# Optimization experiments

Hardware: AMD Instinct MI355X
Metric: run time of the kernel (lower is better)

## Reference

```python
import jax, jax.numpy as jnp
import numpy as np

N_NODES = 100000
N_EDGES = 1600000
N_GRAPHS = 256
F_IN = 128
NEURON = 64
AF = 8  # attention_num_feature


def gcn_conv(h_in, W, b, src, dst, n):
    # PyG GCNConv: add self loops, symmetric normalization, XW then aggregate, + bias
    h = h_in @ W  # [N, out]
    loop = jnp.arange(n)
    s = jnp.concatenate([src, loop])
    d = jnp.concatenate([dst, loop])
    deg = jax.ops.segment_sum(jnp.ones(s.shape[0], h.dtype), d, num_segments=n)
    dis = jax.lax.rsqrt(deg)  # deg >= 1 because of self loops
    norm = dis[s] * dis[d]  # [E+N]
    msg = h[s] * norm[:, None]
    out = jax.ops.segment_sum(msg, d, num_segments=n)
    return out + b


def setup_inputs() -> dict:
    key = jax.random.key(0)
    ks = jax.random.split(key, 16)
    x = jax.random.normal(ks[0], (N_NODES, F_IN), dtype=jnp.float32)
    closeness = jax.random.normal(ks[1], (N_NODES, AF), dtype=jnp.float32)
    edge_index = jax.random.randint(ks[2], (2, N_EDGES), 0, N_NODES, dtype=jnp.int64)
    batch = jnp.sort(jax.random.randint(ks[3], (N_NODES,), 0, N_GRAPHS, dtype=jnp.int64))
    def lin(k, fi, fo):
        lim = 1.0 / np.sqrt(fi)
        return jax.random.uniform(k, (fi, fo), jnp.float32, -lim, lim)
    return {
        "x": x, "closeness": closeness,
        "W1": lin(ks[4], F_IN, NEURON), "b1": jnp.zeros((NEURON,), jnp.float32),
        "W2": lin(ks[5], NEURON, NEURON), "b2": jnp.zeros((NEURON,), jnp.float32),
        "W3": lin(ks[6], NEURON, NEURON), "b3": jnp.zeros((NEURON,), jnp.float32),
        "Wc": lin(ks[7], AF, 1), "bc": jnp.zeros((1,), jnp.float32),
        "Wa1": lin(ks[8], NEURON, 16), "ba1": jnp.zeros((16,), jnp.float32),
        "Wa2": lin(ks[9], 16, 1), "ba2": jnp.zeros((1,), jnp.float32),
        "edge_index": edge_index, "batch": batch,
    }


def reference(x, closeness, W1, b1, W2, b2, W3, b3, Wc, bc, Wa1, ba1, Wa2, ba2, edge_index, batch):
    n, G = x.shape[0], N_GRAPHS
    src, dst = edge_index[0], edge_index[1]
    h = jax.nn.relu(gcn_conv(x, W1, b1, src, dst, n))
    h = jax.nn.relu(gcn_conv(h, W2, b2, src, dst, n))
    h = jax.nn.relu(gcn_conv(h, W3, b3, src, dst, n))  # [N, 64]
    # per-graph softmax over closeness logits (vectorized form of the python loop)
    logits = (closeness @ Wc + bc)[:, 0]  # [N]
    m = jax.ops.segment_max(logits, batch, num_segments=G)
    e = jnp.exp(logits - m[batch])
    z = jax.ops.segment_sum(e, batch, num_segments=G)
    p = e / z[batch]  # softmax within each graph
    counts = jax.ops.segment_sum(jnp.ones((n,), h.dtype), batch, num_segments=G)
    counts = jnp.maximum(counts, 1.0)
    attn = p * counts[batch]  # softmax * curr_size
    # self_average: mean over nodes of attn * h  == segment_sum / count
    g = jax.ops.segment_sum(attn[:, None] * h, batch, num_segments=G) / counts[:, None]  # [G, 64]
    a = jax.nn.relu(g @ Wa1 + ba1)
    return a @ Wa2 + ba2  # [G, 1]
```

## Files before the change

### kernel.cpp

```cpp
#include <hip/hip_runtime.h>
#include <hip/hip_fp16.h>
#include <math.h>


#define BKT_SHIFT 7
#define BKT_NODES 128
#define BKT_CAP 4096
#define EPB 8192

__global__ __launch_bounds__(1024) void block_hist_kernel(
    const int* __restrict__ dst, int* __restrict__ hist, int E, int NBKT, int NBLK) {
  __shared__ int lh[1024];
  const int t = threadIdx.x;
  const int blk = blockIdx.x;
  for (int k = t; k < NBKT; k += 1024) lh[k] = 0;
  __syncthreads();
  const int e0 = blk * EPB;
  const int e1 = min(e0 + EPB, E);
  for (int e = e0 + t; e < e1; e += 1024) atomicAdd(&lh[dst[e] >> BKT_SHIFT], 1);
  __syncthreads();
  for (int k = t; k < NBKT; k += 1024) hist[k * NBLK + blk] = lh[k];
}

__global__ __launch_bounds__(256) void row_scan_kernel(
    const int* __restrict__ hist, int* __restrict__ ebase, int* __restrict__ btot,
    int NBLK) {
  __shared__ int sh[256];
  const int k = blockIdx.x;
  const int t = threadIdx.x;
  int v = (t < NBLK) ? hist[(long)k * NBLK + t] : 0;
  sh[t] = v;
  __syncthreads();
  for (int s = 1; s < 256; s <<= 1) {
    int add = (t >= s) ? sh[t - s] : 0;
    __syncthreads();
    sh[t] += add;
    __syncthreads();
  }
  if (t < NBLK) ebase[(long)k * NBLK + t] = sh[t] - v;
  if (t == 255) btot[k] = sh[255];
}

__global__ __launch_bounds__(1024) void bucket_scan_kernel(
    const int* __restrict__ btot, int* __restrict__ bbase, int E, int NBKT) {
  __shared__ int sh[1024];
  const int t = threadIdx.x;
  int v = (t < NBKT) ? btot[t] : 0;
  sh[t] = v;
  __syncthreads();
  for (int s = 1; s < 1024; s <<= 1) {
    int add = (t >= s) ? sh[t - s] : 0;
    __syncthreads();
    sh[t] += add;
    __syncthreads();
  }
  if (t < NBKT) bbase[t] = sh[t] - v;
  if (t == 0) bbase[NBKT] = E;
}

__global__ __launch_bounds__(1024) void group_kernel(
    const int* __restrict__ src, const int* __restrict__ dst,
    const int* __restrict__ bbase, const int* __restrict__ ebase,
    unsigned int* __restrict__ grouped, int E, int NBKT, int NBLK) {
  __shared__ int lcur[1024];
  const int t = threadIdx.x;
  const int blk = blockIdx.x;
  for (int k = t; k < NBKT; k += 1024)
    lcur[k] = bbase[k] + ebase[(long)k * NBLK + blk];
  __syncthreads();
  const int e0 = blk * EPB;
  const int e1 = min(e0 + EPB, E);
  for (int e = e0 + t; e < e1; e += 1024) {
    int d = dst[e];
    int b = d >> BKT_SHIFT;
    int pos = atomicAdd(&lcur[b], 1);
    grouped[pos] = ((unsigned int)(d & (BKT_NODES - 1)) << 17) | (unsigned int)src[e];
  }
}

__global__ __launch_bounds__(256) void bucket_build_kernel(
    const unsigned int* __restrict__ grouped, const int* __restrict__ bbase,
    int* __restrict__ csr_src, int* __restrict__ ends, float* __restrict__ dis, int N) {
  __shared__ int lcnt[BKT_NODES];
  __shared__ int lsum[BKT_NODES];
  __shared__ int lcur[BKT_NODES];
  __shared__ int stage[BKT_CAP];
  const int b = blockIdx.x;
  const int t = threadIdx.x;
  const int node0 = b << BKT_SHIFT;
  const int nn = min(BKT_NODES, N - node0);
  const int base = bbase[b];
  const int m = bbase[b + 1] - base;

  if (t < BKT_NODES) lcnt[t] = 0;
  __syncthreads();
  for (int i = t; i < m; i += 256) atomicAdd(&lcnt[grouped[base + i] >> 17], 1);
  __syncthreads();
  if (t < BKT_NODES) lsum[t] = lcnt[t];
  __syncthreads();
  for (int s = 1; s < BKT_NODES; s <<= 1) {
    int add = 0;
    if (t < BKT_NODES && t >= s) add = lsum[t - s];
    __syncthreads();
    if (t < BKT_NODES) lsum[t] += add;
    __syncthreads();
  }
  if (t < nn) {
    ends[node0 + t] = base + lsum[t];
    dis[node0 + t] = 1.0f / sqrtf((float)(lcnt[t] + 1));
    lcur[t] = lsum[t] - lcnt[t];
  }
  __syncthreads();
  if (m <= BKT_CAP) {
    for (int i = t; i < m; i += 256) {
      unsigned int v = grouped[base + i];
      int p = atomicAdd(&lcur[v >> 17], 1);
      stage[p] = (int)(v & 0x1FFFFu);
    }
    __syncthreads();
    for (int i = t; i < m; i += 256) csr_src[base + i] = stage[i];
  } else {
    for (int i = t; i < m; i += 256) {
      unsigned int v = grouped[base + i];
      int p = atomicAdd(&lcur[v >> 17], 1);
      csr_src[base + p] = (int)(v & 0x1FFFFu);
    }
  }
}


template <int K>
__global__ __launch_bounds__(256) void gemm_kernel(const float* __restrict__ H,
                                                   const float* __restrict__ W,
                                                   const float* __restrict__ dis,
                                                   __half* __restrict__ C, int N) {
  __shared__ float Hs[64][68];
  __shared__ float Ws[64][64];
  const int t = threadIdx.x;
  const int rowBase = blockIdx.x * 64;
  const int cg = t & 7, pr = t >> 3;
  const int c0 = cg * 8, r0 = pr * 2;
  float acc0[8] = {0.f, 0.f, 0.f, 0.f, 0.f, 0.f, 0.f, 0.f};
  float acc1[8] = {0.f, 0.f, 0.f, 0.f, 0.f, 0.f, 0.f, 0.f};

  const int sr = t >> 4, sc4 = (t & 15) * 4;

  for (int k0 = 0; k0 < K; k0 += 64) {
    __syncthreads();
    {
      const float4* Wv = reinterpret_cast<const float4*>(W + (long)k0 * 64);
#pragma unroll
      for (int i = 0; i < 4; ++i) {
        int idx = t + i * 256;
        *reinterpret_cast<float4*>(&Ws[idx >> 4][(idx & 15) * 4]) = Wv[idx];
      }
    }
#pragma unroll
    for (int i = 0; i < 4; ++i) {
      int r = sr + i * 16;
      int gr = rowBase + r;
      float4 v = make_float4(0.f, 0.f, 0.f, 0.f);
      if (gr < N) v = *reinterpret_cast<const float4*>(H + (long)gr * K + k0 + sc4);
      *reinterpret_cast<float4*>(&Hs[r][sc4]) = v;
    }
    __syncthreads();
#pragma unroll 4
    for (int kk = 0; kk < 64; kk += 4) {
      float4 h0 = *reinterpret_cast<const float4*>(&Hs[r0][kk]);
      float4 h1 = *reinterpret_cast<const float4*>(&Hs[r0 + 1][kk]);
#pragma unroll
      for (int j = 0; j < 4; ++j) {
        float hj0 = (&h0.x)[j];
        float hj1 = (&h1.x)[j];
        const float4 w0 = *reinterpret_cast<const float4*>(&Ws[kk + j][c0]);
        const float4 w1 = *reinterpret_cast<const float4*>(&Ws[kk + j][c0 + 4]);
        acc0[0] += hj0 * w0.x; acc0[1] += hj0 * w0.y; acc0[2] += hj0 * w0.z; acc0[3] += hj0 * w0.w;
        acc0[4] += hj0 * w1.x; acc0[5] += hj0 * w1.y; acc0[6] += hj0 * w1.z; acc0[7] += hj0 * w1.w;
        acc1[0] += hj1 * w0.x; acc1[1] += hj1 * w0.y; acc1[2] += hj1 * w0.z; acc1[3] += hj1 * w0.w;
        acc1[4] += hj1 * w1.x; acc1[5] += hj1 * w1.y; acc1[6] += hj1 * w1.z; acc1[7] += hj1 * w1.w;
      }
    }
  }
  int gr0 = rowBase + r0;
  if (gr0 < N) {
    float s = dis[gr0];
    union { uint4 u; __half2 h[4]; } pk;
    pk.h[0] = __floats2half2_rn(acc0[0] * s, acc0[1] * s);
    pk.h[1] = __floats2half2_rn(acc0[2] * s, acc0[3] * s);
    pk.h[2] = __floats2half2_rn(acc0[4] * s, acc0[5] * s);
    pk.h[3] = __floats2half2_rn(acc0[6] * s, acc0[7] * s);
    *reinterpret_cast<uint4*>(&C[(long)gr0 * 64 + c0]) = pk.u;
  }
  if (gr0 + 1 < N) {
    float s = dis[gr0 + 1];
    union { uint4 u; __half2 h[4]; } pk;
    pk.h[0] = __floats2half2_rn(acc1[0] * s, acc1[1] * s);
    pk.h[1] = __floats2half2_rn(acc1[2] * s, acc1[3] * s);
    pk.h[2] = __floats2half2_rn(acc1[4] * s, acc1[5] * s);
    pk.h[3] = __floats2half2_rn(acc1[6] * s, acc1[7] * s);
    *reinterpret_cast<uint4*>(&C[(long)(gr0 + 1) * 64 + c0]) = pk.u;
  }
}


__device__ __forceinline__ float4 h4_to_f4(uint2 u) {
  const __half2 lo = *reinterpret_cast<const __half2*>(&u.x);
  const __half2 hi = *reinterpret_cast<const __half2*>(&u.y);
  const float2 flo = __half22float2(lo);
  const float2 fhi = __half22float2(hi);
  return make_float4(flo.x, flo.y, fhi.x, fhi.y);
}

__global__ __launch_bounds__(256) void aggregate_kernel(
    const __half* __restrict__ Ts, const int* __restrict__ csr_src,
    const int* __restrict__ ends, const float* __restrict__ dis,
    const float* __restrict__ bias, float* __restrict__ O, int N) {
  int gid = blockIdx.x * 256 + threadIdx.x;
  int d = gid >> 6;
  if (d >= N) return;
  const int lane = threadIdx.x & 63;
  const int q = lane >> 4;
  const int c = lane & 15;
  const int beg = (d == 0) ? 0 : ends[d - 1];
  const int m = ends[d] - beg;
  const uint2* Tv = (const uint2*)Ts;
  const int* sl = csr_src + beg;

  float4 a0 = make_float4(0.f, 0.f, 0.f, 0.f);
  float4 a1 = a0, a2 = a0, a3 = a0;
  if (q == 0) a0 = h4_to_f4(Tv[(long)d * 16 + c]);

  for (int base = 0; base < m; base += 64) {
    const int take = min(m - base, 64);
    int idx = (lane < take) ? sl[base + lane] : 0;
    for (int j = 0; j < take; j += 16) {
      const int l0 = j + q, l1 = j + 4 + q, l2 = j + 8 + q, l3 = j + 12 + q;
      int s0 = __shfl(idx, l0 & 63, 64);
      int s1 = __shfl(idx, l1 & 63, 64);
      int s2 = __shfl(idx, l2 & 63, 64);
      int s3 = __shfl(idx, l3 & 63, 64);
      uint2 r0 = Tv[(long)s0 * 16 + c];
      uint2 r1 = Tv[(long)s1 * 16 + c];
      uint2 r2 = Tv[(long)s2 * 16 + c];
      uint2 r3 = Tv[(long)s3 * 16 + c];
      if (l0 < take) { float4 f = h4_to_f4(r0); a0.x += f.x; a0.y += f.y; a0.z += f.z; a0.w += f.w; }
      if (l1 < take) { float4 f = h4_to_f4(r1); a1.x += f.x; a1.y += f.y; a1.z += f.z; a1.w += f.w; }
      if (l2 < take) { float4 f = h4_to_f4(r2); a2.x += f.x; a2.y += f.y; a2.z += f.z; a2.w += f.w; }
      if (l3 < take) { float4 f = h4_to_f4(r3); a3.x += f.x; a3.y += f.y; a3.z += f.z; a3.w += f.w; }
    }
  }
  a0.x += a1.x; a0.y += a1.y; a0.z += a1.z; a0.w += a1.w;
  a2.x += a3.x; a2.y += a3.y; a2.z += a3.z; a2.w += a3.w;
  a0.x += a2.x; a0.y += a2.y; a0.z += a2.z; a0.w += a2.w;

  a0.x += __shfl_xor(a0.x, 16, 64); a0.y += __shfl_xor(a0.y, 16, 64);
  a0.z += __shfl_xor(a0.z, 16, 64); a0.w += __shfl_xor(a0.w, 16, 64);
  a0.x += __shfl_xor(a0.x, 32, 64); a0.y += __shfl_xor(a0.y, 32, 64);
  a0.z += __shfl_xor(a0.z, 32, 64); a0.w += __shfl_xor(a0.w, 32, 64);

  if (q == 0) {
    float dd = dis[d];
    float4 b4 = ((const float4*)bias)[c];
    float4 o;
    o.x = fmaxf(a0.x * dd + b4.x, 0.f);
    o.y = fmaxf(a0.y * dd + b4.y, 0.f);
    o.z = fmaxf(a0.z * dd + b4.z, 0.f);
    o.w = fmaxf(a0.w * dd + b4.w, 0.f);
    ((float4*)O)[(long)d * 16 + c] = o;
  }
}


__global__ void logits_kernel(const float* __restrict__ clo, const float* __restrict__ Wc,
                              const float* __restrict__ bc, float* __restrict__ lb, int N) {
  int i = blockIdx.x * blockDim.x + threadIdx.x;
  if (i >= N) return;
  float s = bc[0];
#pragma unroll
  for (int k = 0; k < 8; ++k) s += clo[(long)i * 8 + k] * Wc[k];
  lb[i] = s;
}

__global__ __launch_bounds__(256) void pool_kernel(
    const float* __restrict__ h3, const float* __restrict__ lb,
    const int* __restrict__ batch, const float* __restrict__ Wa1,
    const float* __restrict__ ba1, const float* __restrict__ Wa2,
    const float* __restrict__ ba2, float* __restrict__ out, int N) {
  __shared__ int sLo, sHi;
  __shared__ float red[256];
  __shared__ float Vs[4][64];
  __shared__ float sse[4];
  __shared__ float gv[64];
  __shared__ float am[16];
  const int g = blockIdx.x;
  const int t = threadIdx.x;
  if (t == 0) {
    int lo = 0, hi = N;
    while (lo < hi) { int mid = (lo + hi) >> 1; if (batch[mid] < g) lo = mid + 1; else hi = mid; }
    sLo = lo;
    lo = 0; hi = N;
    while (lo < hi) { int mid = (lo + hi) >> 1; if (batch[mid] < g + 1) lo = mid + 1; else hi = mid; }
    sHi = lo;
  }
  __syncthreads();
  const int lo = sLo, hi = sHi;

  float lm = -1e30f;
  for (int i = lo + t; i < hi; i += 256) lm = fmaxf(lm, lb[i]);
  red[t] = lm;
  __syncthreads();
  for (int s = 128; s > 0; s >>= 1) {
    if (t < s) red[t] = fmaxf(red[t], red[t + s]);
    __syncthreads();
  }
  const float m = red[0];

  const int f = t & 63, sub = t >> 6;
  float vacc = 0.f, seacc = 0.f;
  for (int i = lo + sub; i < hi; i += 4) {
    float e = expf(lb[i] - m);
    seacc += e;
    vacc += e * h3[(long)i * 64 + f];
  }
  Vs[sub][f] = vacc;
  if (f == 0) sse[sub] = seacc;
  __syncthreads();
  if (t < 64) {
    float se = sse[0] + sse[1] + sse[2] + sse[3];
    float v = Vs[0][f] + Vs[1][f] + Vs[2][f] + Vs[3][f];
    gv[f] = (se > 0.f) ? v / se : 0.f;
  }
  __syncthreads();
  if (t < 16) {
    float a = ba1[t];
#pragma unroll
    for (int k2 = 0; k2 < 64; ++k2) a += gv[k2] * Wa1[k2 * 16 + t];
    am[t] = a > 0.f ? a : 0.f;
  }
  __syncthreads();
  if (t == 0) {
    float o = ba2[0];
#pragma unroll
    for (int j = 0; j < 16; ++j) o += am[j] * Wa2[j];
    out[g] = o;
  }
}


extern "C" void kernel_launch(void* const* d_in, const int* in_sizes, int n_in,
                              void* d_out, int out_size, void* d_ws, size_t ws_size,
                              hipStream_t stream) {
  const float* x   = (const float*)d_in[0];
  const float* clo = (const float*)d_in[1];
  const float* W1  = (const float*)d_in[2];
  const float* b1  = (const float*)d_in[3];
  const float* W2  = (const float*)d_in[4];
  const float* b2  = (const float*)d_in[5];
  const float* W3  = (const float*)d_in[6];
  const float* b3  = (const float*)d_in[7];
  const float* Wc  = (const float*)d_in[8];
  const float* bc  = (const float*)d_in[9];
  const float* Wa1 = (const float*)d_in[10];
  const float* ba1 = (const float*)d_in[11];
  const float* Wa2 = (const float*)d_in[12];
  const float* ba2 = (const float*)d_in[13];
  const int* edge  = (const int*)d_in[14];
  const int* batch = (const int*)d_in[15];
  float* out = (float*)d_out;

  const int N = in_sizes[15];
  const int E = in_sizes[14] / 2;
  const int G = out_size;
  const int NBKT = (N + BKT_NODES - 1) >> BKT_SHIFT;
  const int NBLK = (E + EPB - 1) / EPB;

  const int* src = edge;
  const int* dst = edge + E;

  char* p = (char*)d_ws;
  auto alloc = [&](size_t bytes) -> char* {
    char* r = p;
    p += (bytes + 255) & ~(size_t)255;
    return r;
  };
  __half* tsbuf         = (__half*)alloc((size_t)N * 64 * sizeof(__half));
  float* bufB           = (float*)alloc((size_t)N * 64 * sizeof(float));
  int*   csr_src        = (int*)  alloc((size_t)E * sizeof(int));
  unsigned int* grouped = (unsigned int*)alloc((size_t)E * sizeof(unsigned int));
  int*   hist           = (int*)  alloc((size_t)NBKT * NBLK * sizeof(int));
  int*   ebase          = (int*)  alloc((size_t)NBKT * NBLK * sizeof(int));
  int*   btot           = (int*)  alloc((size_t)NBKT * sizeof(int));
  int*   bbase          = (int*)  alloc((size_t)(NBKT + 1) * sizeof(int));
  int*   ends           = (int*)  alloc((size_t)N * sizeof(int));
  float* dis            = (float*)alloc((size_t)N * sizeof(float));
  float* lb             = (float*)alloc((size_t)N * sizeof(float));
  (void)ws_size; (void)n_in;

  block_hist_kernel<<<NBLK, 1024, 0, stream>>>(dst, hist, E, NBKT, NBLK);
  row_scan_kernel<<<NBKT, 256, 0, stream>>>(hist, ebase, btot, NBLK);
  bucket_scan_kernel<<<1, 1024, 0, stream>>>(btot, bbase, E, NBKT);
  group_kernel<<<NBLK, 1024, 0, stream>>>(src, dst, bbase, ebase, grouped, E, NBKT, NBLK);
  bucket_build_kernel<<<NBKT, 256, 0, stream>>>(grouped, bbase, csr_src, ends, dis, N);

  const int gN = (N + 255) / 256;
  const int gGemm = (N + 63) / 64;
  const int gAgg  = (N * 64 + 255) / 256;

  gemm_kernel<128><<<gGemm, 256, 0, stream>>>(x, W1, dis, tsbuf, N);
  aggregate_kernel<<<gAgg, 256, 0, stream>>>(tsbuf, csr_src, ends, dis, b1, bufB, N);
  gemm_kernel<64><<<gGemm, 256, 0, stream>>>(bufB, W2, dis, tsbuf, N);
  aggregate_kernel<<<gAgg, 256, 0, stream>>>(tsbuf, csr_src, ends, dis, b2, bufB, N);
  gemm_kernel<64><<<gGemm, 256, 0, stream>>>(bufB, W3, dis, tsbuf, N);
  aggregate_kernel<<<gAgg, 256, 0, stream>>>(tsbuf, csr_src, ends, dis, b3, bufB, N);

  logits_kernel<<<gN, 256, 0, stream>>>(clo, Wc, bc, lb, N);
  pool_kernel<<<G, 256, 0, stream>>>(bufB, lb, batch, Wa1, ba1, Wa2, ba2, out, N);
}
```

Measured before the change: 377.2 us.

## Use MFMA fp16 GEMM and store intermediate activations in half precision

New measurement: 352.0 us. -6.7%, faster.

```diff
diff --git a/kernel.cpp b/kernel.cpp
--- a/kernel.cpp
+++ b/kernel.cpp
@@ -7,6 +7,9 @@
 #define BKT_NODES 128
 #define BKT_CAP 4096
 #define EPB 8192
+
+typedef _Float16 f16x8 __attribute__((ext_vector_type(8)));
+typedef float f32x4 __attribute__((ext_vector_type(4)));
 
 __global__ __launch_bounds__(1024) void block_hist_kernel(
     const int* __restrict__ dst, int* __restrict__ hist, int E, int NBKT, int NBLK) {
@@ -129,76 +132,102 @@
 }
 
 
-template <int K>
-__global__ __launch_bounds__(256) void gemm_kernel(const float* __restrict__ H,
-                                                   const float* __restrict__ W,
-                                                   const float* __restrict__ dis,
-                                                   __half* __restrict__ C, int N) {
-  __shared__ float Hs[64][68];
-  __shared__ float Ws[64][64];
+template <int K, typename Tin>
+__global__ __launch_bounds__(256) void gemm_mfma_kernel(
+    const Tin* __restrict__ H, const float* __restrict__ W,
+    const float* __restrict__ dis, __half* __restrict__ C, int N) {
+  __shared__ __align__(16) __half Hs[64 * K];
+  __shared__ __align__(16) __half Ws[64 * K];
   const int t = threadIdx.x;
   const int rowBase = blockIdx.x * 64;
-  const int cg = t & 7, pr = t >> 3;
-  const int c0 = cg * 8, r0 = pr * 2;
-  float acc0[8] = {0.f, 0.f, 0.f, 0.f, 0.f, 0.f, 0.f, 0.f};
-  float acc1[8] = {0.f, 0.f, 0.f, 0.f, 0.f, 0.f, 0.f, 0.f};
-
-  const int sr = t >> 4, sc4 = (t & 15) * 4;
-
-  for (int k0 = 0; k0 < K; k0 += 64) {
-    __syncthreads();
-    {
-      const float4* Wv = reinterpret_cast<const float4*>(W + (long)k0 * 64);
-#pragma unroll
-      for (int i = 0; i < 4; ++i) {
-        int idx = t + i * 256;
-        *reinterpret_cast<float4*>(&Ws[idx >> 4][(idx & 15) * 4]) = Wv[idx];
+
+  if constexpr (sizeof(Tin) == 4) {
+    const int NF4 = 64 * K / 4;
+#pragma unroll
+    for (int i = 0; i < NF4 / 256; ++i) {
+      int f = t + i * 256;
+      int row = f / (K / 4);
+      int c4 = f % (K / 4);
+      int gr = rowBase + row;
+      float4 v = make_float4(0.f, 0.f, 0.f, 0.f);
+      if (gr < N) v = *reinterpret_cast<const float4*>(H + (long)gr * K + c4 * 4);
+      union { uint2 u; __half2 h[2]; } pk;
+      pk.h[0] = __floats2half2_rn(v.x, v.y);
+      pk.h[1] = __floats2half2_rn(v.z, v.w);
+      int byte = (row * K + c4 * 4) * 2;
+      byte ^= (row & 7) << 4;
+      *reinterpret_cast<uint2*>(reinterpret_cast<char*>(Hs) + byte) = pk.u;
+    }
+  } else {
+    const int NC = 64 * K / 8;
+#pragma unroll
+    for (int i = 0; i < NC / 256; ++i) {
+      int f = t + i * 256;
+      int row = f / (K / 8);
+      int c8 = f % (K / 8);
+      int gr = rowBase + row;
+      uint4 v = make_uint4(0u, 0u, 0u, 0u);
+      if (gr < N) v = *reinterpret_cast<const uint4*>(H + (long)gr * K + c8 * 8);
+      int byte = (row * K + c8 * 8) * 2;
+      byte ^= (row & 7) << 4;
+      *reinterpret_cast<uint4*>(reinterpret_cast<char*>(Hs) + byte) = v;
+    }
+  }
+
+  {
+    const int NU = (K / 2) * 16;
+#pragma unroll
+    for (int i = 0; i < NU / 256; ++i) {
+      int u = t + i * 256;
+      int kp = u >> 4;
+      int cq = u & 15;
+      const float4 w0 = *reinterpret_cast<const float4*>(W + (long)(2 * kp) * 64 + cq * 4);
+      const float4 w1 = *reinterpret_cast<const float4*>(W + (long)(2 * kp + 1) * 64 + cq * 4);
+#pragma unroll
+      for (int j = 0; j < 4; ++j) {
+        int c = cq * 4 + j;
+        __half2 p = __floats2half2_rn((&w0.x)[j], (&w1.x)[j]);
+        int byte = (c * K + 2 * kp) * 2;
+        byte ^= (c & 7) << 4;
+        *reinterpret_cast<__half2*>(reinterpret_cast<char*>(Ws) + byte) = p;
       }
     }
-#pragma unroll
-    for (int i = 0; i < 4; ++i) {
-      int r = sr + i * 16;
-      int gr = rowBase + r;
-      float4 v = make_float4(0.f, 0.f, 0.f, 0.f);
-      if (gr < N) v = *reinterpret_cast<const float4*>(H + (long)gr * K + k0 + sc4);
-      *reinterpret_cast<float4*>(&Hs[r][sc4]) = v;
-    }
-    __syncthreads();
-#pragma unroll 4
-    for (int kk = 0; kk < 64; kk += 4) {
-      float4 h0 = *reinterpret_cast<const float4*>(&Hs[r0][kk]);
-      float4 h1 = *reinterpret_cast<const float4*>(&Hs[r0 + 1][kk]);
-#pragma unroll
-      for (int j = 0; j < 4; ++j) {
-        float hj0 = (&h0.x)[j];
-        float hj1 = (&h1.x)[j];
-        const float4 w0 = *reinterpret_cast<const float4*>(&Ws[kk + j][c0]);
-        const float4 w1 = *reinterpret_cast<const float4*>(&Ws[kk + j][c0 + 4]);
-        acc0[0] += hj0 * w0.x; acc0[1] += hj0 * w0.y; acc0[2] += hj0 * w0.z; acc0[3] += hj0 * w0.w;
-        acc0[4] += hj0 * w1.x; acc0[5] += hj0 * w1.y; acc0[6] += hj0 * w1.z; acc0[7] += hj0 * w1.w;
-        acc1[0] += hj1 * w0.x; acc1[1] += hj1 * w0.y; acc1[2] += hj1 * w0.z; acc1[3] += hj1 * w0.w;
-        acc1[4] += hj1 * w1.x; acc1[5] += hj1 * w1.y; acc1[6] += hj1 * w1.z; acc1[7] += hj1 * w1.w;
+  }
+  __syncthreads();
+
+  const int w = t >> 6;
+  const int l = t & 63;
+  const int r = l & 15;
+  const int g = l >> 4;
+  const int rowL = 16 * w + r;
+  f32x4 acc[4] = {{0.f, 0.f, 0.f, 0.f}, {0.f, 0.f, 0.f, 0.f},
+                  {0.f, 0.f, 0.f, 0.f}, {0.f, 0.f, 0.f, 0.f}};
+#pragma unroll
+  for (int s = 0; s < K / 32; ++s) {
+    int abyte = (rowL * K + s * 32 + g * 8) * 2;
+    abyte ^= (rowL & 7) << 4;
+    f16x8 afrag = *reinterpret_cast<const f16x8*>(reinterpret_cast<const char*>(Hs) + abyte);
+#pragma unroll
+    for (int n = 0; n < 4; ++n) {
+      int col = n * 16 + r;
+      int bbyte = (col * K + s * 32 + g * 8) * 2;
+      bbyte ^= (col & 7) << 4;
+      f16x8 bfrag = *reinterpret_cast<const f16x8*>(reinterpret_cast<const char*>(Ws) + bbyte);
+      acc[n] = __builtin_amdgcn_mfma_f32_16x16x32_f16(afrag, bfrag, acc[n], 0, 0, 0);
+    }
+  }
+
+  const int outRow0 = rowBase + 16 * w + 4 * g;
+#pragma unroll
+  for (int j = 0; j < 4; ++j) {
+    int row = outRow0 + j;
+    if (row < N) {
+      float dv = dis[row];
+#pragma unroll
+      for (int n = 0; n < 4; ++n) {
+        C[(long)row * 64 + n * 16 + r] = __float2half(acc[n][j] * dv);
       }
     }
-  }
-  int gr0 = rowBase + r0;
-  if (gr0 < N) {
-    float s = dis[gr0];
-    union { uint4 u; __half2 h[4]; } pk;
-    pk.h[0] = __floats2half2_rn(acc0[0] * s, acc0[1] * s);
-    pk.h[1] = __floats2half2_rn(acc0[2] * s, acc0[3] * s);
-    pk.h[2] = __floats2half2_rn(acc0[4] * s, acc0[5] * s);
-    pk.h[3] = __floats2half2_rn(acc0[6] * s, acc0[7] * s);
-    *reinterpret_cast<uint4*>(&C[(long)gr0 * 64 + c0]) = pk.u;
-  }
-  if (gr0 + 1 < N) {
-    float s = dis[gr0 + 1];
-    union { uint4 u; __half2 h[4]; } pk;
-    pk.h[0] = __floats2half2_rn(acc1[0] * s, acc1[1] * s);
-    pk.h[1] = __floats2half2_rn(acc1[2] * s, acc1[3] * s);
-    pk.h[2] = __floats2half2_rn(acc1[4] * s, acc1[5] * s);
-    pk.h[3] = __floats2half2_rn(acc1[6] * s, acc1[7] * s);
-    *reinterpret_cast<uint4*>(&C[(long)(gr0 + 1) * 64 + c0]) = pk.u;
   }
 }
 
@@ -214,7 +243,7 @@
 __global__ __launch_bounds__(256) void aggregate_kernel(
     const __half* __restrict__ Ts, const int* __restrict__ csr_src,
     const int* __restrict__ ends, const float* __restrict__ dis,
-    const float* __restrict__ bias, float* __restrict__ O, int N) {
+    const float* __restrict__ bias, __half* __restrict__ O, int N) {
   int gid = blockIdx.x * 256 + threadIdx.x;
   int d = gid >> 6;
   if (d >= N) return;
@@ -261,12 +290,10 @@
   if (q == 0) {
     float dd = dis[d];
     float4 b4 = ((const float4*)bias)[c];
-    float4 o;
-    o.x = fmaxf(a0.x * dd + b4.x, 0.f);
-    o.y = fmaxf(a0.y * dd + b4.y, 0.f);
-    o.z = fmaxf(a0.z * dd + b4.z, 0.f);
-    o.w = fmaxf(a0.w * dd + b4.w, 0.f);
-    ((float4*)O)[(long)d * 16 + c] = o;
+    union { uint2 u; __half2 h[2]; } pk;
+    pk.h[0] = __floats2half2_rn(fmaxf(a0.x * dd + b4.x, 0.f), fmaxf(a0.y * dd + b4.y, 0.f));
+    pk.h[1] = __floats2half2_rn(fmaxf(a0.z * dd + b4.z, 0.f), fmaxf(a0.w * dd + b4.w, 0.f));
+    ((uint2*)O)[(long)d * 16 + c] = pk.u;
   }
 }
 
@@ -282,7 +309,7 @@
 }
 
 __global__ __launch_bounds__(256) void pool_kernel(
-    const float* __restrict__ h3, const float* __restrict__ lb,
+    const __half* __restrict__ h3, const float* __restrict__ lb,
     const int* __restrict__ batch, const float* __restrict__ Wa1,
     const float* __restrict__ ba1, const float* __restrict__ Wa2,
     const float* __restrict__ ba2, float* __restrict__ out, int N) {
@@ -320,7 +347,7 @@
   for (int i = lo + sub; i < hi; i += 4) {
     float e = expf(lb[i] - m);
     seacc += e;
-    vacc += e * h3[(long)i * 64 + f];
+    vacc += e * __half2float(h3[(long)i * 64 + f]);
   }
   Vs[sub][f] = vacc;
   if (f == 0) sse[sub] = seacc;
@@ -384,7 +411,7 @@
     return r;
   };
   __half* tsbuf         = (__half*)alloc((size_t)N * 64 * sizeof(__half));
-  float* bufB           = (float*)alloc((size_t)N * 64 * sizeof(float));
+  __half* bufH          = (__half*)alloc((size_t)N * 64 * sizeof(__half));
   int*   csr_src        = (int*)  alloc((size_t)E * sizeof(int));
   unsigned int* grouped = (unsigned int*)alloc((size_t)E * sizeof(unsigned int));
   int*   hist           = (int*)  alloc((size_t)NBKT * NBLK * sizeof(int));
@@ -406,13 +433,13 @@
   const int gGemm = (N + 63) / 64;
   const int gAgg  = (N * 64 + 255) / 256;
 
-  gemm_kernel<128><<<gGemm, 256, 0, stream>>>(x, W1, dis, tsbuf, N);
-  aggregate_kernel<<<gAgg, 256, 0, stream>>>(tsbuf, csr_src, ends, dis, b1, bufB, N);
-  gemm_kernel<64><<<gGemm, 256, 0, stream>>>(bufB, W2, dis, tsbuf, N);
-  aggregate_kernel<<<gAgg, 256, 0, stream>>>(tsbuf, csr_src, ends, dis, b2, bufB, N);
-  gemm_kernel<64><<<gGemm, 256, 0, stream>>>(bufB, W3, dis, tsbuf, N);
-  aggregate_kernel<<<gAgg, 256, 0, stream>>>(tsbuf, csr_src, ends, dis, b3, bufB, N);
+  gemm_mfma_kernel<128, float><<<gGemm, 256, 0, stream>>>(x, W1, dis, tsbuf, N);
+  aggregate_kernel<<<gAgg, 256, 0, stream>>>(tsbuf, csr_src, ends, dis, b1, bufH, N);
+  gemm_mfma_kernel<64, __half><<<gGemm, 256, 0, stream>>>(bufH, W2, dis, tsbuf, N);
+  aggregate_kernel<<<gAgg, 256, 0, stream>>>(tsbuf, csr_src, ends, dis, b2, bufH, N);
+  gemm_mfma_kernel<64, __half><<<gGemm, 256, 0, stream>>>(bufH, W3, dis, tsbuf, N);
+  aggregate_kernel<<<gAgg, 256, 0, stream>>>(tsbuf, csr_src, ends, dis, b3, bufH, N);
 
   logits_kernel<<<gN, 256, 0, stream>>>(clo, Wc, bc, lb, N);
-  pool_kernel<<<G, 256, 0, stream>>>(bufB, lb, batch, Wa1, ba1, Wa2, ba2, out, N);
-}
+  pool_kernel<<<G, 256, 0, stream>>>(bufH, lb, batch, Wa1, ba1, Wa2, ba2, out, N);
+}
```
